# Kernel optimization log

Hardware: AMD Instinct MI355X
Metric: run time of the kernel (lower is better)

The kernel has to match this reference:

```python
import jax, jax.numpy as jnp
import numpy as np

TOP_K = 2  # config.n_expert_per_token


def setup_inputs() -> dict:
    key = jax.random.key(0)
    ks = jax.random.split(key, 5)
    B, T, C, E, F = 2, 2048, 2048, 8, 1024
    scale = 0.02
    return {
        "x": jax.random.normal(ks[0], (B, T, C), jnp.float32),
        "w_router": jax.random.normal(ks[1], (C, E), jnp.float32) * scale,
        "w1": jax.random.normal(ks[2], (E, C, F), jnp.float32) * scale,  # fc_1 (gate proj)
        "w3": jax.random.normal(ks[3], (E, C, F), jnp.float32) * scale,  # fc_2 (up proj)
        "w2": jax.random.normal(ks[4], (E, F, C), jnp.float32) * scale,  # proj (down)
    }


def reference(x, w_router, w1, w3, w2):
    B, T, C = x.shape
    xt = x.reshape(-1, C)                                  # [N, C]
    N = xt.shape[0]
    E = w_router.shape[1]
    # Router: topk logits, softmax over the selected k in fp32
    logits = xt @ w_router                                 # [N, E]
    top_vals, top_idx = jax.lax.top_k(logits, TOP_K)       # [N, k]
    probs = jax.nn.softmax(top_vals.astype(jnp.float32), axis=1).astype(xt.dtype)
    # Per-token per-expert combine weight (0 for unselected experts).
    # topk indices are distinct per token, so scatter-add == scatter-set.
    w = jnp.zeros((N, E), xt.dtype).at[jnp.arange(N)[:, None], top_idx].add(probs)  # [N, E]
    # Dense grouped SwiGLU expert MLPs; zero-weight tokens contribute nothing.
    g = jnp.einsum('nc,ecf->enf', xt, w1)                  # [E, N, F]
    u = jnp.einsum('nc,ecf->enf', xt, w3)                  # [E, N, F]
    h = jax.nn.silu(g) * u                                 # [E, N, F]
    outs = jnp.einsum('enf,efc->enc', h, w2)               # [E, N, C]
    y = jnp.einsum('enc,ne->nc', outs, w)                  # weighted combine
    return y.reshape(B, T, C)
```

## Files before the change

### kernel.cpp

```cpp
#include <hip/hip_runtime.h>
#include <hip/hip_bf16.h>
#include <stdint.h>

#define N_TOK 4096
#define CDIM 2048
#define EXP 8
#define FDIM 1024
#define LDSTRIDE 40

typedef __attribute__((ext_vector_type(4))) float f32x4;
typedef __attribute__((ext_vector_type(8))) short bf16x8;

__global__ __launch_bounds__(256) void transpose_to_bf16(
    const float* __restrict__ in, __hip_bfloat16* __restrict__ out, int R, int Cc) {
  __shared__ float tile[64][65];
  int e = blockIdx.z;
  const float* ip = in + (size_t)e * R * Cc;
  __hip_bfloat16* op = out + (size_t)e * R * Cc;
  int r0 = blockIdx.y * 64, c0 = blockIdx.x * 64;
  int t = threadIdx.x;
  {
    int r = t >> 2, cb = (t & 3) * 16;
    const float* src = ip + (size_t)(r0 + r) * Cc + c0 + cb;
#pragma unroll
    for (int i = 0; i < 4; i++) {
      float4 v = *(const float4*)(src + i * 4);
      tile[cb + i * 4 + 0][r] = v.x;
      tile[cb + i * 4 + 1][r] = v.y;
      tile[cb + i * 4 + 2][r] = v.z;
      tile[cb + i * 4 + 3][r] = v.w;
    }
  }
  __syncthreads();
  {
    int c = t >> 2, sb = (t & 3) * 16;
    union { int4 v[2]; __hip_bfloat16 h[16]; } u;
#pragma unroll
    for (int j = 0; j < 16; j++) u.h[j] = __float2bfloat16(tile[c][sb + j]);
    __hip_bfloat16* dst = op + (size_t)(c0 + c) * R + r0 + sb;
    *(int4*)(dst) = u.v[0];
    *(int4*)(dst + 8) = u.v[1];
  }
}

__global__ __launch_bounds__(256) void router_kernel(
    const float* __restrict__ x, const float* __restrict__ wr,
    __hip_bfloat16* __restrict__ x_bf, int* __restrict__ counts,
    int* __restrict__ pair_expert, float* __restrict__ pair_prob) {
  int tok = blockIdx.x;
  const float* xr = x + (size_t)tok * CDIM;
  int t = threadIdx.x;
  float acc[EXP];
#pragma unroll
  for (int e = 0; e < EXP; e++) acc[e] = 0.f;
#pragma unroll
  for (int j = 0; j < 8; j++) {
    int c = j * 256 + t;
    float xv = xr[c];
    x_bf[(size_t)tok * CDIM + c] = __float2bfloat16(xv);
    const float4* wr4 = (const float4*)(wr + (size_t)c * EXP);
    float4 wa = wr4[0], wb = wr4[1];
    acc[0] += xv * wa.x; acc[1] += xv * wa.y; acc[2] += xv * wa.z; acc[3] += xv * wa.w;
    acc[4] += xv * wb.x; acc[5] += xv * wb.y; acc[6] += xv * wb.z; acc[7] += xv * wb.w;
  }
#pragma unroll
  for (int e = 0; e < EXP; e++) {
#pragma unroll
    for (int off = 32; off > 0; off >>= 1) acc[e] += __shfl_down(acc[e], off, 64);
  }
  __shared__ float wsum[4][EXP];
  int wid = t >> 6, lane = t & 63;
  if (lane == 0) {
#pragma unroll
    for (int e = 0; e < EXP; e++) wsum[wid][e] = acc[e];
  }
  __syncthreads();
  if (t == 0) {
    float lg[EXP];
#pragma unroll
    for (int e = 0; e < EXP; e++) lg[e] = wsum[0][e] + wsum[1][e] + wsum[2][e] + wsum[3][e];
    int i0 = 0;
#pragma unroll
    for (int e = 1; e < EXP; e++) if (lg[e] > lg[i0]) i0 = e;
    int i1 = (i0 == 0) ? 1 : 0;
#pragma unroll
    for (int e = 0; e < EXP; e++) if (e != i0 && lg[e] > lg[i1]) i1 = e;
    float e1 = __expf(lg[i1] - lg[i0]);
    float p0 = 1.f / (1.f + e1);
    pair_expert[tok * 2 + 0] = i0;
    pair_expert[tok * 2 + 1] = i1;
    pair_prob[tok * 2 + 0] = p0;
    pair_prob[tok * 2 + 1] = e1 * p0;
    atomicAdd(&counts[i0], 1);
    atomicAdd(&counts[i1], 1);
  }
}

__global__ void scan_kernel(const int* __restrict__ counts, int* __restrict__ bases) {
  if (threadIdx.x == 0) {
    int s = 0;
    for (int e = 0; e < EXP; e++) { bases[e] = s; s += counts[e]; }
  }
}

__global__ __launch_bounds__(256) void scatter_kernel(
    const int* __restrict__ pair_expert, const int* __restrict__ bases,
    int* __restrict__ cursors, int* __restrict__ lists) {
  int tok = blockIdx.x * 256 + threadIdx.x;
  if (tok >= N_TOK) return;
#pragma unroll
  for (int k = 0; k < 2; k++) {
    int e = pair_expert[tok * 2 + k];
    int pos = atomicAdd(&cursors[e], 1);
    lists[bases[e] + pos] = tok * 2 + k;
  }
}

__global__ __launch_bounds__(256) void gemm1_kernel(
    const __hip_bfloat16* __restrict__ xbf, const __hip_bfloat16* __restrict__ w1t,
    const __hip_bfloat16* __restrict__ w3t, const int* __restrict__ counts,
    const int* __restrict__ bases, const int* __restrict__ lists,
    __hip_bfloat16* __restrict__ h) {
  int e = blockIdx.z;
  int n_e = counts[e];
  int m0 = blockIdx.y * 128;
  if (m0 >= n_e) return;
  int base = bases[e];
  int f0 = blockIdx.x * 64;

  __shared__ short As[128 * LDSTRIDE];
  __shared__ short B1s[64 * LDSTRIDE];
  __shared__ short B3s[64 * LDSTRIDE];

  int t = threadIdx.x;
  int lane = t & 63, wid = t >> 6;

  int arow = t >> 1;
  int achunk = (t & 1) * 16;
  int rr = m0 + arow;
  int pair = lists[base + ((rr < n_e) ? rr : 0)];
  int tokA = pair >> 1;

  const short* xs = (const short*)xbf;
  const short* b1p = (const short*)w1t + (size_t)e * FDIM * CDIM;
  const short* b3p = (const short*)w3t + (size_t)e * FDIM * CDIM;
  int brow = (t & 127) >> 1;
  bool doB1 = (t < 128);
  const short* bsrc = (doB1 ? b1p : b3p) + (size_t)(f0 + brow) * CDIM + achunk;
  short* bdst = (doB1 ? B1s : B3s) + brow * LDSTRIDE + achunk;
  const short* asrc = xs + (size_t)tokA * CDIM + achunk;
  short* adst = As + arow * LDSTRIDE + achunk;

  int4 pa0 = *(const int4*)(asrc);
  int4 pa1 = *(const int4*)(asrc + 8);
  int4 pb0 = *(const int4*)(bsrc);
  int4 pb1 = *(const int4*)(bsrc + 8);

  f32x4 zero = {0.f, 0.f, 0.f, 0.f};
  f32x4 accg[4][2], accu[4][2];
#pragma unroll
  for (int i = 0; i < 4; i++)
#pragma unroll
    for (int j = 0; j < 2; j++) { accg[i][j] = zero; accu[i][j] = zero; }

  int wm = (wid & 1) * 64, wf = (wid >> 1) * 32;
  int kq = (lane >> 4) * 8;
  int rsel = lane & 15;

  for (int kk = 0; kk < CDIM; kk += 32) {
    __syncthreads();
    *(int4*)(adst) = pa0;
    *(int4*)(adst + 8) = pa1;
    *(int4*)(bdst) = pb0;
    *(int4*)(bdst + 8) = pb1;
    __syncthreads();
    if (kk + 32 < CDIM) {
      pa0 = *(const int4*)(asrc + kk + 32);
      pa1 = *(const int4*)(asrc + kk + 40);
      pb0 = *(const int4*)(bsrc + kk + 32);
      pb1 = *(const int4*)(bsrc + kk + 40);
    }
    bf16x8 af[4], b1f[2], b3f[2];
#pragma unroll
    for (int i = 0; i < 4; i++)
      af[i] = *(const bf16x8*)(As + (wm + i * 16 + rsel) * LDSTRIDE + kq);
#pragma unroll
    for (int j = 0; j < 2; j++) {
      b1f[j] = *(const bf16x8*)(B1s + (wf + j * 16 + rsel) * LDSTRIDE + kq);
      b3f[j] = *(const bf16x8*)(B3s + (wf + j * 16 + rsel) * LDSTRIDE + kq);
    }
#pragma unroll
    for (int i = 0; i < 4; i++)
#pragma unroll
      for (int j = 0; j < 2; j++) {
        accg[i][j] = __builtin_amdgcn_mfma_f32_16x16x32_bf16(af[i], b1f[j], accg[i][j], 0, 0, 0);
        accu[i][j] = __builtin_amdgcn_mfma_f32_16x16x32_bf16(af[i], b3f[j], accu[i][j], 0, 0, 0);
      }
  }

  int col = lane & 15;
  int rbase = (lane >> 4) * 4;
#pragma unroll
  for (int i = 0; i < 4; i++) {
#pragma unroll
    for (int r = 0; r < 4; r++) {
      int m = m0 + wm + i * 16 + rbase + r;
      if (m < n_e) {
        size_t hrow = (size_t)(base + m) * FDIM;
#pragma unroll
        for (int j = 0; j < 2; j++) {
          int f = f0 + wf + j * 16 + col;
          float g = accg[i][j][r];
          float u = accu[i][j][r];
          float sg = g / (1.f + __expf(-g));
          h[hrow + f] = __float2bfloat16(sg * u);
        }
      }
    }
  }
}

__global__ __launch_bounds__(256) void gemm2_kernel(
    const __hip_bfloat16* __restrict__ h, const __hip_bfloat16* __restrict__ w2t,
    const int* __restrict__ counts, const int* __restrict__ bases,
    const int* __restrict__ lists, const float* __restrict__ pair_prob,
    float* __restrict__ out) {
  int e = blockIdx.z;
  int n_e = counts[e];
  int m0 = blockIdx.y * 128;
  if (m0 >= n_e) return;
  int base = bases[e];
  int c0 = blockIdx.x * 128;

  __shared__ short As[128 * LDSTRIDE];
  __shared__ short Bs[128 * LDSTRIDE];

  int t = threadIdx.x;
  int lane = t & 63, wid = t >> 6;

  int arow = t >> 1;
  int achunk = (t & 1) * 16;
  int hr = base + m0 + arow;
  if (hr > 2 * N_TOK - 1) hr = 2 * N_TOK - 1;
  const short* hp = (const short*)h;
  const short* bp = (const short*)w2t + (size_t)e * CDIM * FDIM;
  const short* asrc = hp + (size_t)hr * FDIM + achunk;
  const short* bsrc = bp + (size_t)(c0 + arow) * FDIM + achunk;
  short* adst = As + arow * LDSTRIDE + achunk;
  short* bdst = Bs + arow * LDSTRIDE + achunk;

  int4 pa0 = *(const int4*)(asrc);
  int4 pa1 = *(const int4*)(asrc + 8);
  int4 pb0 = *(const int4*)(bsrc);
  int4 pb1 = *(const int4*)(bsrc + 8);

  f32x4 zero = {0.f, 0.f, 0.f, 0.f};
  f32x4 acc[4][4];
#pragma unroll
  for (int i = 0; i < 4; i++)
#pragma unroll
    for (int j = 0; j < 4; j++) acc[i][j] = zero;

  int wm = (wid & 1) * 64, wn = (wid >> 1) * 64;
  int kq = (lane >> 4) * 8;
  int rsel = lane & 15;

  for (int kk = 0; kk < FDIM; kk += 32) {
    __syncthreads();
    *(int4*)(adst) = pa0;
    *(int4*)(adst + 8) = pa1;
    *(int4*)(bdst) = pb0;
    *(int4*)(bdst + 8) = pb1;
    __syncthreads();
    if (kk + 32 < FDIM) {
      pa0 = *(const int4*)(asrc + kk + 32);
      pa1 = *(const int4*)(asrc + kk + 40);
      pb0 = *(const int4*)(bsrc + kk + 32);
      pb1 = *(const int4*)(bsrc + kk + 40);
    }
    bf16x8 af[4], bfr[4];
#pragma unroll
    for (int i = 0; i < 4; i++)
      af[i] = *(const bf16x8*)(As + (wm + i * 16 + rsel) * LDSTRIDE + kq);
#pragma unroll
    for (int j = 0; j < 4; j++)
      bfr[j] = *(const bf16x8*)(Bs + (wn + j * 16 + rsel) * LDSTRIDE + kq);
#pragma unroll
    for (int i = 0; i < 4; i++)
#pragma unroll
      for (int j = 0; j < 4; j++)
        acc[i][j] = __builtin_amdgcn_mfma_f32_16x16x32_bf16(af[i], bfr[j], acc[i][j], 0, 0, 0);
  }

  int col = lane & 15;
  int rbase = (lane >> 4) * 4;
#pragma unroll
  for (int i = 0; i < 4; i++) {
#pragma unroll
    for (int r = 0; r < 4; r++) {
      int m = m0 + wm + i * 16 + rbase + r;
      if (m < n_e) {
        int pr = lists[base + m];
        int tok = pr >> 1;
        float p = pair_prob[pr];
        size_t orow = (size_t)tok * CDIM;
#pragma unroll
        for (int j = 0; j < 4; j++) {
          int c = c0 + wn + j * 16 + col;
          atomicAdd(&out[orow + c], acc[i][j][r] * p);
        }
      }
    }
  }
}

extern "C" void kernel_launch(void* const* d_in, const int* in_sizes, int n_in,
                              void* d_out, int out_size, void* d_ws, size_t ws_size,
                              hipStream_t stream) {
  const float* x  = (const float*)d_in[0];
  const float* wr = (const float*)d_in[1];
  const float* w1 = (const float*)d_in[2];
  const float* w3 = (const float*)d_in[3];
  const float* w2 = (const float*)d_in[4];
  float* out = (float*)d_out;

  char* ws = (char*)d_ws;
  __hip_bfloat16* x_bf = (__hip_bfloat16*)(ws);
  __hip_bfloat16* h    = (__hip_bfloat16*)(ws + 16777216);
  __hip_bfloat16* w1t  = (__hip_bfloat16*)(ws + 33554432);
  __hip_bfloat16* w3t  = (__hip_bfloat16*)(ws + 67108864);
  __hip_bfloat16* w2t  = (__hip_bfloat16*)(ws + 100663296);
  int* counts  = (int*)(ws + 134217728);
  int* bases   = counts + 8;
  int* cursors = counts + 16;
  int* pair_expert = (int*)(ws + 134217728 + 128);
  float* pair_prob = (float*)(ws + 134217728 + 128 + 32768);
  int* lists       = (int*)(ws + 134217728 + 128 + 65536);

  hipMemsetAsync(d_out, 0, (size_t)N_TOK * CDIM * sizeof(float), stream);
  hipMemsetAsync(counts, 0, 128, stream);

  transpose_to_bf16<<<dim3(FDIM / 64, CDIM / 64, EXP), 256, 0, stream>>>(w1, w1t, CDIM, FDIM);
  transpose_to_bf16<<<dim3(FDIM / 64, CDIM / 64, EXP), 256, 0, stream>>>(w3, w3t, CDIM, FDIM);
  transpose_to_bf16<<<dim3(CDIM / 64, FDIM / 64, EXP), 256, 0, stream>>>(w2, w2t, FDIM, CDIM);

  router_kernel<<<N_TOK, 256, 0, stream>>>(x, wr, x_bf, counts, pair_expert, pair_prob);
  scan_kernel<<<1, 64, 0, stream>>>(counts, bases);
  scatter_kernel<<<N_TOK / 256, 256, 0, stream>>>(pair_expert, bases, cursors, lists);

  gemm1_kernel<<<dim3(FDIM / 64, N_TOK / 128, EXP), 256, 0, stream>>>(
      x_bf, w1t, w3t, counts, bases, lists, h);
  gemm2_kernel<<<dim3(CDIM / 128, N_TOK / 128, EXP), 256, 0, stream>>>(
      h, w2t, counts, bases, lists, pair_prob, out);
}
```

Measured before the change: 624.2 us.

## Use direct global-to-LDS loads and replace atomic combine with separate combine kernel

GEMM tile loads now use global_load_lds to move data directly into unpadded LDS, replacing register-staged loads with software prefetch. The down-projection no longer atomically accumulates weighted results into the output. It writes per-slot fp32 rows into a workspace that reuses the transposed-weight region, and a new combine kernel sums the two expert rows per token with their probabilities. This removes the output memset and the atomic contention, at the cost of extra fp32 traffic, lost load/compute overlap, and possible LDS bank conflicts from the unpadded stride.

```diff
diff --git a/kernel.cpp b/kernel.cpp
--- a/kernel.cpp
+++ b/kernel.cpp
@@ -6,10 +6,15 @@
 #define CDIM 2048
 #define EXP 8
 #define FDIM 1024
-#define LDSTRIDE 40
 
 typedef __attribute__((ext_vector_type(4))) float f32x4;
 typedef __attribute__((ext_vector_type(8))) short bf16x8;
+
+__device__ __forceinline__ void gl2lds16(const short* g, short* l) {
+  __builtin_amdgcn_global_load_lds(
+      (const __attribute__((address_space(1))) void*)g,
+      (__attribute__((address_space(3))) void*)l, 16, 0, 0);
+}
 
 __global__ __launch_bounds__(256) void transpose_to_bf16(
     const float* __restrict__ in, __hip_bfloat16* __restrict__ out, int R, int Cc) {
@@ -105,14 +110,16 @@
 
 __global__ __launch_bounds__(256) void scatter_kernel(
     const int* __restrict__ pair_expert, const int* __restrict__ bases,
-    int* __restrict__ cursors, int* __restrict__ lists) {
+    int* __restrict__ cursors, int* __restrict__ lists, int* __restrict__ slot_map) {
   int tok = blockIdx.x * 256 + threadIdx.x;
   if (tok >= N_TOK) return;
 #pragma unroll
   for (int k = 0; k < 2; k++) {
     int e = pair_expert[tok * 2 + k];
     int pos = atomicAdd(&cursors[e], 1);
-    lists[bases[e] + pos] = tok * 2 + k;
+    int slot = bases[e] + pos;
+    lists[slot] = tok * 2 + k;
+    slot_map[tok * 2 + k] = slot;
   }
 }
 
@@ -128,33 +135,28 @@
   int base = bases[e];
   int f0 = blockIdx.x * 64;
 
-  __shared__ short As[128 * LDSTRIDE];
-  __shared__ short B1s[64 * LDSTRIDE];
-  __shared__ short B3s[64 * LDSTRIDE];
+  __shared__ short As[128 * 32];
+  __shared__ short B1s[64 * 32];
+  __shared__ short B3s[64 * 32];
 
   int t = threadIdx.x;
   int lane = t & 63, wid = t >> 6;
 
-  int arow = t >> 1;
-  int achunk = (t & 1) * 16;
-  int rr = m0 + arow;
-  int pair = lists[base + ((rr < n_e) ? rr : 0)];
-  int tokA = pair >> 1;
+  int rowA = t >> 2, sub = (t & 3) * 8;
+  int r1 = m0 + rowA, r2 = m0 + 64 + rowA;
+  int tok1 = lists[base + ((r1 < n_e) ? r1 : 0)] >> 1;
+  int tok2 = lists[base + ((r2 < n_e) ? r2 : 0)] >> 1;
 
   const short* xs = (const short*)xbf;
-  const short* b1p = (const short*)w1t + (size_t)e * FDIM * CDIM;
-  const short* b3p = (const short*)w3t + (size_t)e * FDIM * CDIM;
-  int brow = (t & 127) >> 1;
-  bool doB1 = (t < 128);
-  const short* bsrc = (doB1 ? b1p : b3p) + (size_t)(f0 + brow) * CDIM + achunk;
-  short* bdst = (doB1 ? B1s : B3s) + brow * LDSTRIDE + achunk;
-  const short* asrc = xs + (size_t)tokA * CDIM + achunk;
-  short* adst = As + arow * LDSTRIDE + achunk;
-
-  int4 pa0 = *(const int4*)(asrc);
-  int4 pa1 = *(const int4*)(asrc + 8);
-  int4 pb0 = *(const int4*)(bsrc);
-  int4 pb1 = *(const int4*)(bsrc + 8);
+  const short* ag1 = xs + (size_t)tok1 * CDIM + sub;
+  const short* ag2 = xs + (size_t)tok2 * CDIM + sub;
+  const short* b1g = (const short*)w1t + (size_t)e * FDIM * CDIM + (size_t)(f0 + rowA) * CDIM + sub;
+  const short* b3g = (const short*)w3t + (size_t)e * FDIM * CDIM + (size_t)(f0 + rowA) * CDIM + sub;
+
+  short* al1 = As + wid * 512;
+  short* al2 = As + 2048 + wid * 512;
+  short* b1l = B1s + wid * 512;
+  short* b3l = B3s + wid * 512;
 
   f32x4 zero = {0.f, 0.f, 0.f, 0.f};
   f32x4 accg[4][2], accu[4][2];
@@ -169,25 +171,19 @@
 
   for (int kk = 0; kk < CDIM; kk += 32) {
     __syncthreads();
-    *(int4*)(adst) = pa0;
-    *(int4*)(adst + 8) = pa1;
-    *(int4*)(bdst) = pb0;
-    *(int4*)(bdst + 8) = pb1;
+    gl2lds16(ag1 + kk, al1);
+    gl2lds16(ag2 + kk, al2);
+    gl2lds16(b1g + kk, b1l);
+    gl2lds16(b3g + kk, b3l);
     __syncthreads();
-    if (kk + 32 < CDIM) {
-      pa0 = *(const int4*)(asrc + kk + 32);
-      pa1 = *(const int4*)(asrc + kk + 40);
-      pb0 = *(const int4*)(bsrc + kk + 32);
-      pb1 = *(const int4*)(bsrc + kk + 40);
-    }
     bf16x8 af[4], b1f[2], b3f[2];
 #pragma unroll
     for (int i = 0; i < 4; i++)
-      af[i] = *(const bf16x8*)(As + (wm + i * 16 + rsel) * LDSTRIDE + kq);
+      af[i] = *(const bf16x8*)(As + (wm + i * 16 + rsel) * 32 + kq);
 #pragma unroll
     for (int j = 0; j < 2; j++) {
-      b1f[j] = *(const bf16x8*)(B1s + (wf + j * 16 + rsel) * LDSTRIDE + kq);
-      b3f[j] = *(const bf16x8*)(B3s + (wf + j * 16 + rsel) * LDSTRIDE + kq);
+      b1f[j] = *(const bf16x8*)(B1s + (wf + j * 16 + rsel) * 32 + kq);
+      b3f[j] = *(const bf16x8*)(B3s + (wf + j * 16 + rsel) * 32 + kq);
     }
 #pragma unroll
     for (int i = 0; i < 4; i++)
@@ -223,8 +219,7 @@
 __global__ __launch_bounds__(256) void gemm2_kernel(
     const __hip_bfloat16* __restrict__ h, const __hip_bfloat16* __restrict__ w2t,
     const int* __restrict__ counts, const int* __restrict__ bases,
-    const int* __restrict__ lists, const float* __restrict__ pair_prob,
-    float* __restrict__ out) {
+    float* __restrict__ o_pair) {
   int e = blockIdx.z;
   int n_e = counts[e];
   int m0 = blockIdx.y * 128;
@@ -232,27 +227,28 @@
   int base = bases[e];
   int c0 = blockIdx.x * 128;
 
-  __shared__ short As[128 * LDSTRIDE];
-  __shared__ short Bs[128 * LDSTRIDE];
+  __shared__ short As[128 * 32];
+  __shared__ short Bs[128 * 32];
 
   int t = threadIdx.x;
   int lane = t & 63, wid = t >> 6;
 
-  int arow = t >> 1;
-  int achunk = (t & 1) * 16;
-  int hr = base + m0 + arow;
-  if (hr > 2 * N_TOK - 1) hr = 2 * N_TOK - 1;
+  int rowA = t >> 2, sub = (t & 3) * 8;
+  int hr1 = base + m0 + rowA;
+  int hr2 = base + m0 + 64 + rowA;
+  if (hr1 > 2 * N_TOK - 1) hr1 = 2 * N_TOK - 1;
+  if (hr2 > 2 * N_TOK - 1) hr2 = 2 * N_TOK - 1;
   const short* hp = (const short*)h;
   const short* bp = (const short*)w2t + (size_t)e * CDIM * FDIM;
-  const short* asrc = hp + (size_t)hr * FDIM + achunk;
-  const short* bsrc = bp + (size_t)(c0 + arow) * FDIM + achunk;
-  short* adst = As + arow * LDSTRIDE + achunk;
-  short* bdst = Bs + arow * LDSTRIDE + achunk;
-
-  int4 pa0 = *(const int4*)(asrc);
-  int4 pa1 = *(const int4*)(asrc + 8);
-  int4 pb0 = *(const int4*)(bsrc);
-  int4 pb1 = *(const int4*)(bsrc + 8);
+  const short* ag1 = hp + (size_t)hr1 * FDIM + sub;
+  const short* ag2 = hp + (size_t)hr2 * FDIM + sub;
+  const short* bg1 = bp + (size_t)(c0 + rowA) * FDIM + sub;
+  const short* bg2 = bp + (size_t)(c0 + 64 + rowA) * FDIM + sub;
+
+  short* al1 = As + wid * 512;
+  short* al2 = As + 2048 + wid * 512;
+  short* bl1 = Bs + wid * 512;
+  short* bl2 = Bs + 2048 + wid * 512;
 
   f32x4 zero = {0.f, 0.f, 0.f, 0.f};
   f32x4 acc[4][4];
@@ -267,24 +263,18 @@
 
   for (int kk = 0; kk < FDIM; kk += 32) {
     __syncthreads();
-    *(int4*)(adst) = pa0;
-    *(int4*)(adst + 8) = pa1;
-    *(int4*)(bdst) = pb0;
-    *(int4*)(bdst + 8) = pb1;
+    gl2lds16(ag1 + kk, al1);
+    gl2lds16(ag2 + kk, al2);
+    gl2lds16(bg1 + kk, bl1);
+    gl2lds16(bg2 + kk, bl2);
     __syncthreads();
-    if (kk + 32 < FDIM) {
-      pa0 = *(const int4*)(asrc + kk + 32);
-      pa1 = *(const int4*)(asrc + kk + 40);
-      pb0 = *(const int4*)(bsrc + kk + 32);
-      pb1 = *(const int4*)(bsrc + kk + 40);
-    }
     bf16x8 af[4], bfr[4];
 #pragma unroll
     for (int i = 0; i < 4; i++)
-      af[i] = *(const bf16x8*)(As + (wm + i * 16 + rsel) * LDSTRIDE + kq);
+      af[i] = *(const bf16x8*)(As + (wm + i * 16 + rsel) * 32 + kq);
 #pragma unroll
     for (int j = 0; j < 4; j++)
-      bfr[j] = *(const bf16x8*)(Bs + (wn + j * 16 + rsel) * LDSTRIDE + kq);
+      bfr[j] = *(const bf16x8*)(Bs + (wn + j * 16 + rsel) * 32 + kq);
 #pragma unroll
     for (int i = 0; i < 4; i++)
 #pragma unroll
@@ -300,17 +290,37 @@
     for (int r = 0; r < 4; r++) {
       int m = m0 + wm + i * 16 + rbase + r;
       if (m < n_e) {
-        int pr = lists[base + m];
-        int tok = pr >> 1;
-        float p = pair_prob[pr];
-        size_t orow = (size_t)tok * CDIM;
+        size_t orow = (size_t)(base + m) * CDIM;
 #pragma unroll
         for (int j = 0; j < 4; j++) {
           int c = c0 + wn + j * 16 + col;
-          atomicAdd(&out[orow + c], acc[i][j][r] * p);
+          o_pair[orow + c] = acc[i][j][r];
         }
       }
     }
+  }
+}
+
+__global__ __launch_bounds__(256) void combine_kernel(
+    const float* __restrict__ o_pair, const int* __restrict__ slot_map,
+    const float* __restrict__ pair_prob, float* __restrict__ out) {
+  int tok = blockIdx.x;
+  int s0 = slot_map[tok * 2 + 0], s1 = slot_map[tok * 2 + 1];
+  float p0 = pair_prob[tok * 2 + 0], p1 = pair_prob[tok * 2 + 1];
+  const float4* r0 = (const float4*)(o_pair + (size_t)s0 * CDIM);
+  const float4* r1 = (const float4*)(o_pair + (size_t)s1 * CDIM);
+  float4* op = (float4*)(out + (size_t)tok * CDIM);
+  int t = threadIdx.x;
+#pragma unroll
+  for (int j = 0; j < 2; j++) {
+    int i = j * 256 + t;
+    float4 a = r0[i], b = r1[i];
+    float4 c;
+    c.x = p0 * a.x + p1 * b.x;
+    c.y = p0 * a.y + p1 * b.y;
+    c.z = p0 * a.z + p1 * b.z;
+    c.w = p0 * a.w + p1 * b.w;
+    op[i] = c;
   }
 }
 
@@ -330,14 +340,15 @@
   __hip_bfloat16* w1t  = (__hip_bfloat16*)(ws + 33554432);
   __hip_bfloat16* w3t  = (__hip_bfloat16*)(ws + 67108864);
   __hip_bfloat16* w2t  = (__hip_bfloat16*)(ws + 100663296);
+  float* o_pair = (float*)(ws + 33554432);
   int* counts  = (int*)(ws + 134217728);
   int* bases   = counts + 8;
   int* cursors = counts + 16;
   int* pair_expert = (int*)(ws + 134217728 + 128);
   float* pair_prob = (float*)(ws + 134217728 + 128 + 32768);
   int* lists       = (int*)(ws + 134217728 + 128 + 65536);
-
-  hipMemsetAsync(d_out, 0, (size_t)N_TOK * CDIM * sizeof(float), stream);
+  int* slot_map    = (int*)(ws + 134217728 + 128 + 98304);
+
   hipMemsetAsync(counts, 0, 128, stream);
 
   transpose_to_bf16<<<dim3(FDIM / 64, CDIM / 64, EXP), 256, 0, stream>>>(w1, w1t, CDIM, FDIM);
@@ -346,10 +357,11 @@
 
   router_kernel<<<N_TOK, 256, 0, stream>>>(x, wr, x_bf, counts, pair_expert, pair_prob);
   scan_kernel<<<1, 64, 0, stream>>>(counts, bases);
-  scatter_kernel<<<N_TOK / 256, 256, 0, stream>>>(pair_expert, bases, cursors, lists);
+  scatter_kernel<<<N_TOK / 256, 256, 0, stream>>>(pair_expert, bases, cursors, lists, slot_map);
 
   gemm1_kernel<<<dim3(FDIM / 64, N_TOK / 128, EXP), 256, 0, stream>>>(
       x_bf, w1t, w3t, counts, bases, lists, h);
   gemm2_kernel<<<dim3(CDIM / 128, N_TOK / 128, EXP), 256, 0, stream>>>(
-      h, w2t, counts, bases, lists, pair_prob, out);
-}
+      h, w2t, counts, bases, o_pair);
+  combine_kernel<<<N_TOK, 256, 0, stream>>>(o_pair, slot_map, pair_prob, out);
+}
```

New measurement: 618.5 us. Within noise of the previous version (-0.9%).
